# Kernel optimization log

Measured on AMD Instinct MI355X. Metric: run time of the kernel, lower is better.

Reference implementation:

```python
import jax, jax.numpy as jnp
import numpy as np

N = 50000      # nodes per graph
E = 800000     # edges per graph (avg degree 16)
IN = 128       # in_channels == hidden_channels
HID = 128      # out_channels (heads=1)
R = 8          # num_relations
NEG = 0.2      # PyG RGATConv default negative_slope


def setup_inputs() -> dict:
    key = jax.random.key(0)
    ks = jax.random.split(key, 14)
    s_w = (2.0 / (IN + HID)) ** 0.5  # glorot-ish scale
    return {
        "x_one": jax.random.normal(ks[0], (N, IN), jnp.float32),
        "edge_index_one": jax.random.randint(ks[1], (2, E), 0, N),
        "edge_type_one": jax.random.randint(ks[2], (E,), 0, R),
        "x_two": jax.random.normal(ks[3], (N, IN), jnp.float32),
        "edge_index_two": jax.random.randint(ks[4], (2, E), 0, N),
        "edge_type_two": jax.random.randint(ks[5], (E,), 0, R),
        "W1": jax.random.normal(ks[6], (R, IN, HID), jnp.float32) * s_w,
        "q1": jax.random.normal(ks[7], (HID, 1), jnp.float32) * s_w,
        "k1": jax.random.normal(ks[8], (HID, 1), jnp.float32) * s_w,
        "b1": jnp.zeros((HID,), jnp.float32),
        "W2": jax.random.normal(ks[9], (R, IN, HID), jnp.float32) * s_w,
        "q2": jax.random.normal(ks[10], (HID, 1), jnp.float32) * s_w,
        "k2": jax.random.normal(ks[11], (HID, 1), jnp.float32) * s_w,
        "b2": jnp.zeros((HID,), jnp.float32),
    }


def _rgat(x, edge_index, edge_type, W, q, k, b):
    """PyG RGATConv (heads=1, additive-self-attention, across-relation)."""
    n = x.shape[0]
    src, dst = edge_index[0], edge_index[1]
    # per-relation linear transform of all nodes: [R, N, HID]
    xt = jnp.einsum('nd,rdo->rno', x, W)
    out_i = xt[edge_type, dst]   # [E, HID] transformed target (x_i W_r)
    out_j = xt[edge_type, src]   # [E, HID] transformed source (x_j W_r)
    qi = out_i @ q               # [E, 1]
    kj = out_j @ k               # [E, 1]
    alpha = jax.nn.leaky_relu(qi + kj, NEG)
    # scatter-softmax over incoming edges of each dst node
    amax = jax.ops.segment_max(alpha, dst, num_segments=n)
    amax = jnp.where(jnp.isfinite(amax), amax, 0.0)
    ex = jnp.exp(alpha - amax[dst])
    denom = jax.ops.segment_sum(ex, dst, num_segments=n) + 1e-16
    a = ex / denom[dst]          # [E, 1]
    # weighted scatter-add aggregation + bias
    out = jax.ops.segment_sum(a * out_j, dst, num_segments=n) + b
    return out


def reference(x_one, edge_index_one, edge_type_one,
              x_two, edge_index_two, edge_type_two,
              W1, q1, k1, b1, W2, q2, k2, b2):
    o1 = jax.nn.relu(_rgat(x_one, edge_index_one, edge_type_one, W1, q1, k1, b1))
    o2 = jax.nn.relu(_rgat(x_two, edge_index_two, edge_type_two, W2, q2, k2, b2))
    return (o1, o2)
```

## Files before the change

### kernel.cpp

```cpp
#include <hip/hip_runtime.h>


typedef unsigned short u16;
typedef __attribute__((ext_vector_type(8))) short short8;
typedef __attribute__((ext_vector_type(4))) float floatx4;
typedef __attribute__((ext_vector_type(4))) float float4v;
typedef __attribute__((ext_vector_type(4))) unsigned uint4v;

__device__ __forceinline__ u16 f2bf(float f) {
  union { float f; unsigned u; } v; v.f = f;
  unsigned r = v.u + 0x7FFFu + ((v.u >> 16) & 1u);
  return (u16)(r >> 16);
}
__device__ __forceinline__ float bflo(unsigned v) {
  union { unsigned u; float f; } c; c.u = v << 16; return c.f;
}
__device__ __forceinline__ float bfhi(unsigned v) {
  union { unsigned u; float f; } c; c.u = v & 0xffff0000u; return c.f;
}
__device__ __forceinline__ unsigned cvtpk(float lo, float hi) {
  unsigned r;
  asm("v_cvt_pk_bf16_f32 %0, %1, %2" : "=v"(r) : "v"(lo), "v"(hi));
  return r;
}

__global__ void k_prep_wb(const float* __restrict__ W1, const float* __restrict__ W2,
                          u16* __restrict__ Wb, int KK) {
  int t = blockIdx.x * 256 + threadIdx.x;
  int lane = t & 63, nt = (t >> 6) & 7, kk = t >> 9;
  if (kk >= KK) return;
  const float* W = blockIdx.y ? W2 : W1;
  u16* out = Wb + (size_t)blockIdx.y * KK * 4096;
  int q = lane >> 4, m16 = lane & 15;
  int c = nt * 16 + m16;
  short8 v;
#pragma unroll
  for (int j = 0; j < 8; ++j) {
    int k = kk * 32 + q * 8 + j;
    v[j] = (short)f2bf(W[(size_t)k * 128 + c]);
  }
  *(short8*)(out + (size_t)t * 8) = v;
}

__global__ void __launch_bounds__(256) k_prep_bqk(
    const float* __restrict__ W1, const float* __restrict__ q1,
    const float* __restrict__ k1, const float* __restrict__ W2,
    const float* __restrict__ q2, const float* __restrict__ k2,
    u16* __restrict__ Bqk) {
  int idx = blockIdx.x * 256 + threadIdx.x;
  int j = idx & 7, lane = (idx >> 3) & 63, kk = (idx >> 9) & 3, g = idx >> 11;
  int k = kk * 32 + ((lane >> 4) & 3) * 8 + j;
  int n = lane & 15;
  const float* W = g ? W2 : W1;
  const float* vec = (n < 8) ? (g ? q2 : q1) : (g ? k2 : k1);
  const float* row = W + ((size_t)(n & 7) * 128 + k) * 128;
  float s = 0.f;
#pragma unroll
  for (int o = 0; o < 128; o += 4) {
    float4v wv = *(const float4v*)(row + o);
    float4v qv = *(const float4v*)(vec + o);
    s += wv.x * qv.x + wv.y * qv.y + wv.z * qv.z + wv.w * qv.w;
  }
  Bqk[idx] = f2bf(s);
}

__global__ void __launch_bounds__(256) k_count(
    const int* __restrict__ d1, const int* __restrict__ d2,
    int* __restrict__ gcnt, int N, int E, int NB) {
  __shared__ int h[512];
  int tid = threadIdx.x;
  for (int i = tid; i < NB; i += 256) h[i] = 0;
  __syncthreads();
  int E2 = 2 * E;
  int e0 = blockIdx.x * 4096;
#pragma unroll
  for (int j = 0; j < 16; ++j) {
    int e = e0 + j * 256 + tid;
    if (e < E2) {
      int g = e >= E;
      int d = g ? d2[e - E] : d1[e];
      atomicAdd(&h[(g * N + d) >> 8], 1);
    }
  }
  __syncthreads();
  for (int i = tid; i < NB; i += 256)
    if (h[i]) atomicAdd(&gcnt[i], h[i]);
}

__global__ void k_bucket_scan(const int* __restrict__ gcnt, int* __restrict__ bbase,
                              int* __restrict__ bcur, int* __restrict__ offs,
                              int NB, int total, int N2) {
  __shared__ int sd[512];
  int tid = threadIdx.x;
  int v0 = (tid < NB) ? gcnt[tid] : 0;
  int v1 = (tid + 256 < NB) ? gcnt[tid + 256] : 0;
  sd[tid] = v0; sd[tid + 256] = v1;
  __syncthreads();
  for (int off = 1; off < 512; off <<= 1) {
    int t0 = (tid >= off) ? sd[tid - off] : 0;
    int t1 = (tid + 256 >= off) ? sd[tid + 256 - off] : 0;
    __syncthreads();
    sd[tid] += t0; sd[tid + 256] += t1;
    __syncthreads();
  }
  if (tid < NB) { int b = sd[tid] - v0; bbase[tid] = b; bcur[tid] = b; }
  if (tid + 256 < NB) { int b = sd[tid + 256] - v1; bbase[tid + 256] = b; bcur[tid + 256] = b; }
  if (tid == 0) { bbase[NB] = total; offs[N2] = total; }
}

__global__ void __launch_bounds__(256) k_bin(
    const int* __restrict__ ei1, const int* __restrict__ et1,
    const int* __restrict__ ei2, const int* __restrict__ et2,
    int* __restrict__ bcur, uint2* __restrict__ staged, int N, int E, int NB) {
  __shared__ int hist[512];
  __shared__ int basev[512];
  __shared__ int runstart[512];
  __shared__ unsigned sta[4096 * 2];
  int tid = threadIdx.x;
  int E2 = 2 * E;
  int e0 = blockIdx.x * 4096;
  int cnt2 = min(4096, E2 - e0);
  for (int i = tid; i < 512; i += 256) hist[i] = 0;
  __syncthreads();
  int dstg[16], srcet[16], rank[16];
#pragma unroll
  for (int j = 0; j < 16; ++j) {
    int e = e0 + j * 256 + tid;
    dstg[j] = -1;
    if (e < E2) {
      int g = e >= E;
      int el = e - (g ? E : 0);
      const int* ei = g ? ei2 : ei1;
      int s = ei[el], d = ei[E + el];
      int etv = (g ? et2 : et1)[el];
      dstg[j] = g * N + d;
      srcet[j] = (s << 3) | etv;
      rank[j] = atomicAdd(&hist[dstg[j] >> 8], 1);
    }
  }
  __syncthreads();
  basev[tid] = hist[tid];
  basev[tid + 256] = hist[tid + 256];
  __syncthreads();
  for (int off = 1; off < 512; off <<= 1) {
    int i0 = tid, i1 = tid + 256;
    int v0 = (i0 >= off) ? basev[i0 - off] : 0;
    int v1 = (i1 >= off) ? basev[i1 - off] : 0;
    __syncthreads();
    basev[i0] += v0; basev[i1] += v1;
    __syncthreads();
  }
  for (int i = tid; i < NB; i += 256)
    if (hist[i] > 0) runstart[i] = atomicAdd(&bcur[i], hist[i]);
  __syncthreads();
#pragma unroll
  for (int j = 0; j < 16; ++j)
    if (dstg[j] >= 0) {
      int b = dstg[j] >> 8;
      int slot = basev[b] - hist[b] + rank[j];
      sta[slot * 2] = (unsigned)dstg[j];
      sta[slot * 2 + 1] = (unsigned)srcet[j];
    }
  __syncthreads();
  for (int i = tid; i < cnt2; i += 256) {
    unsigned dg = sta[i * 2], se = sta[i * 2 + 1];
    int b = (int)(dg >> 8);
    int dest = runstart[b] + (i - (basev[b] - hist[b]));
    staged[dest] = make_uint2(dg, se);
  }
}

__global__ void __launch_bounds__(256) k_scatter2(
    const uint2* __restrict__ staged, const int* __restrict__ bbase,
    int* __restrict__ offs, int* __restrict__ csr, int N2) {
  __shared__ int hist[256];
  __shared__ int sd[256];
  __shared__ int cur[256];
  int b = blockIdx.x, tid = threadIdx.x;
  int nb0 = b << 8;
  int nnode = min(256, N2 - nb0);
  int s0 = bbase[b], s1 = bbase[b + 1];
  hist[tid] = 0;
  __syncthreads();
  for (int i = s0 + tid; i < s1; i += 256)
    atomicAdd(&hist[(int)staged[i].x - nb0], 1);
  __syncthreads();
  int v = hist[tid];
  sd[tid] = v; __syncthreads();
  for (int off = 1; off < 256; off <<= 1) {
    int t = (tid >= off) ? sd[tid - off] : 0;
    __syncthreads();
    sd[tid] += t;
    __syncthreads();
  }
  int ex = sd[tid] - v;
  if (tid < nnode) offs[nb0 + tid] = s0 + ex;
  cur[tid] = ex;
  __syncthreads();
  for (int i = s0 + tid; i < s1; i += 256) {
    uint2 en = staged[i];
    int node = (int)en.x - nb0;
    int sl = atomicAdd(&cur[node], 1);
    csr[s0 + sl] = (int)en.y;
  }
}

__global__ void __launch_bounds__(256) k_gemm_xt(
    const float* __restrict__ x1, const float* __restrict__ x2,
    const u16* __restrict__ Wb, const u16* __restrict__ Bqk,
    u16* __restrict__ xt, unsigned long long xt_gstride,
    float* __restrict__ sq, float* __restrict__ sk,
    int N, int R, int g0) {
  __shared__ u16 st[4][2][2048];
  int g = g0 + blockIdx.z;
  const float* x = g ? x2 : x1;
  const u16* Wbg = Wb + (size_t)g * (R * 4) * 4096;
  const u16* Bqkg = Bqk + (size_t)g * 2048;
  u16* xtg = xt + (size_t)g * xt_gstride;
  int node_base = g * N;
  int wave = threadIdx.x >> 6, lane = threadIdx.x & 63;
  int m0 = blockIdx.x * 64 + wave * 16;
  int rbase = blockIdx.y * 4;
  int q = lane >> 4, m16 = lane & 15;
  int node = m0 + m16;
  int srow = (node < N) ? node : N - 1;
  short8 bfrag[4];
#pragma unroll
  for (int kk = 0; kk < 4; ++kk) {
    const float* ap = x + (size_t)srow * 128 + kk * 32 + q * 8;
    float4v f0 = *(const float4v*)ap;
    float4v f1 = *(const float4v*)(ap + 4);
    union { unsigned u[4]; short8 s; } pb;
    pb.u[0] = cvtpk(f0.x, f0.y); pb.u[1] = cvtpk(f0.z, f0.w);
    pb.u[2] = cvtpk(f1.x, f1.y); pb.u[3] = cvtpk(f1.z, f1.w);
    bfrag[kk] = pb.s;
  }
  if (blockIdx.y == 0) {
    floatx4 accq = (floatx4){0.f, 0.f, 0.f, 0.f};
#pragma unroll
    for (int kk = 0; kk < 4; ++kk) {
      short8 aq = *(const short8*)(Bqkg + (size_t)kk * 512 + lane * 8);
      accq = __builtin_amdgcn_mfma_f32_16x16x32_bf16(aq, bfrag[kk], accq, 0, 0, 0);
    }
    if (node < N) {
      float* dst = (q < 2 ? sq : sk) + (size_t)(node_base + node) * 8 + (q & 1) * 4;
      *(float4v*)dst = (float4v){accq[0], accq[1], accq[2], accq[3]};
    }
  }
#pragma unroll
  for (int rr = 0; rr < 4; ++rr) {
    int r = rbase + rr;
    u16* s = st[wave][rr & 1];
    floatx4 acc[8];
#pragma unroll
    for (int nt = 0; nt < 8; ++nt) acc[nt] = (floatx4){0.f, 0.f, 0.f, 0.f};
#pragma unroll
    for (int kk = 0; kk < 4; ++kk) {
      const u16* wbp = Wbg + ((size_t)((r * 4 + kk) * 8) * 64 + lane) * 8;
#pragma unroll
      for (int nt = 0; nt < 8; ++nt) {
        short8 a = *(const short8*)(wbp + nt * 512);
        acc[nt] = __builtin_amdgcn_mfma_f32_16x16x32_bf16(a, bfrag[kk], acc[nt], 0, 0, 0);
      }
    }
#pragma unroll
    for (int nt = 0; nt < 8; ++nt) {
      union { unsigned u[2]; unsigned long long ull; } pk;
      pk.u[0] = cvtpk(acc[nt][0], acc[nt][1]);
      pk.u[1] = cvtpk(acc[nt][2], acc[nt][3]);
      int c16 = 2 * nt + (q >> 1);
      *(unsigned long long*)(s + (((m16 << 4) + (c16 ^ m16)) << 3) + ((q & 1) << 2)) = pk.ull;
    }
#pragma unroll
    for (int it = 0; it < 4; ++it) {
      int rl = it * 4 + q;
      int gm = m0 + rl;
      if (gm < N) {
        uint4v vv = *(const uint4v*)(s + (((rl << 4) + (m16 ^ rl)) << 3));
        *(uint4v*)(xtg + ((size_t)r * N + gm) * 128 + m16 * 8) = vv;
      }
    }
  }
}

__global__ void __launch_bounds__(256) k_aggregate(
    const int* __restrict__ csr, const int* __restrict__ offs,
    const float* __restrict__ sq, const float* __restrict__ sk,
    const u16* __restrict__ xt, unsigned long long xt_gstride,
    const float* __restrict__ b1, const float* __restrict__ b2,
    float* __restrict__ out, int N, int g0) {
  int nl = blockIdx.x * 4 + (threadIdx.x >> 6);
  int lane = threadIdx.x & 63;
  if (nl >= N) return;
  int g = g0 + blockIdx.y;
  int node_base = g * N;
  const float* bias = g ? b2 : b1;
  const u16* xtg = xt + (size_t)g * xt_gstride;
  float* outp = out + (size_t)g * N * 128;
  int node = node_base + nl;
  int start = offs[node], end = offs[node + 1];
  const float* sqn = sq + (size_t)node * 8;

  float al[8]; int pl[8];
  float m = -INFINITY;
  {
    int c = 0;
    for (int i = start + lane; i < end; i += 64, ++c) {
      int p = csr[i]; int s = p >> 3, e = p & 7;
      float a = sqn[e] + sk[(size_t)(node_base + s) * 8 + e];
      a = (a > 0.f) ? a : 0.2f * a;
      if (c < 8) { al[c] = a; pl[c] = p; }
      m = fmaxf(m, a);
    }
  }
#pragma unroll
  for (int off = 32; off; off >>= 1) m = fmaxf(m, __shfl_xor(m, off));

  float ssum = 0.f;
  {
    int c = 0;
    for (int i = start + lane; i < end; i += 64, ++c) {
      float a;
      if (c < 8) a = al[c];
      else {
        int p = csr[i]; int s = p >> 3, e = p & 7;
        a = sqn[e] + sk[(size_t)(node_base + s) * 8 + e];
        a = (a > 0.f) ? a : 0.2f * a;
      }
      ssum += __expf(a - m);
    }
  }
#pragma unroll
  for (int off = 32; off; off >>= 1) ssum += __shfl_xor(ssum, off);
  float inv = 1.f / (ssum + 1e-16f);

  float acc0 = 0.f, acc1 = 0.f;
  const char* xtb = (const char*)xtg;
  int c = 0;
  for (int base = start; base < end; base += 64, ++c) {
    int cnt = min(64, end - base);
    float w = 0.f; int b = 0;
    {
      int i = base + lane;
      if (i < end) {
        int p; float a;
        if (c < 8) { p = pl[c]; a = al[c]; }
        else {
          p = csr[i]; int s = p >> 3, e = p & 7;
          a = sqn[e] + sk[(size_t)(node_base + s) * 8 + e];
          a = (a > 0.f) ? a : 0.2f * a;
        }
        w = __expf(a - m) * inv;
        b = ((p & 7) * N + (p >> 3)) << 8;
      }
    }
    int j = 0;
    for (; j + 3 < cnt; j += 4) {
      float w0 = __shfl(w, j), w1 = __shfl(w, j + 1),
            w2 = __shfl(w, j + 2), w3 = __shfl(w, j + 3);
      int b0 = __shfl(b, j), b1_ = __shfl(b, j + 1),
          b2_ = __shfl(b, j + 2), b3 = __shfl(b, j + 3);
      unsigned v0 = *(const unsigned*)(xtb + b0 + lane * 4);
      unsigned v1 = *(const unsigned*)(xtb + b1_ + lane * 4);
      unsigned v2 = *(const unsigned*)(xtb + b2_ + lane * 4);
      unsigned v3 = *(const unsigned*)(xtb + b3 + lane * 4);
      acc0 += w0 * bflo(v0); acc1 += w0 * bfhi(v0);
      acc0 += w1 * bflo(v1); acc1 += w1 * bfhi(v1);
      acc0 += w2 * bflo(v2); acc1 += w2 * bfhi(v2);
      acc0 += w3 * bflo(v3); acc1 += w3 * bfhi(v3);
    }
    for (; j < cnt; ++j) {
      float w0 = __shfl(w, j);
      int b0 = __shfl(b, j);
      unsigned v0 = *(const unsigned*)(xtb + b0 + lane * 4);
      acc0 += w0 * bflo(v0); acc1 += w0 * bfhi(v0);
    }
  }
  float o0 = fmaxf(acc0 + bias[lane * 2], 0.f);
  float o1 = fmaxf(acc1 + bias[lane * 2 + 1], 0.f);
  union { float f[2]; unsigned long long u; } pk;
  pk.f[0] = o0; pk.f[1] = o1;
  __builtin_nontemporal_store(pk.u,
      (unsigned long long*)(outp + (size_t)nl * 128 + lane * 2));
}

extern "C" void kernel_launch(void* const* d_in, const int* in_sizes, int n_in,
                              void* d_out, int out_size, void* d_ws, size_t ws_size,
                              hipStream_t stream) {
  const float* x1 = (const float*)d_in[0];
  const int* ei1 = (const int*)d_in[1];
  const int* et1 = (const int*)d_in[2];
  const float* x2 = (const float*)d_in[3];
  const int* ei2 = (const int*)d_in[4];
  const int* et2 = (const int*)d_in[5];
  const float* W1 = (const float*)d_in[6];
  const float* q1 = (const float*)d_in[7];
  const float* k1 = (const float*)d_in[8];
  const float* b1 = (const float*)d_in[9];
  const float* W2 = (const float*)d_in[10];
  const float* q2 = (const float*)d_in[11];
  const float* k2 = (const float*)d_in[12];
  const float* b2 = (const float*)d_in[13];

  const int N = in_sizes[0] / 128;
  const int E = in_sizes[1] / 2;
  const int R = in_sizes[6] / (128 * 128);
  const int KK = R * 4;
  const int N2 = 2 * N;
  const int NB = (N2 + 255) >> 8;

  size_t off = 0;
  char* w = (char*)d_ws;
  auto carve = [&](size_t bytes) -> void* {
    void* p = w + off;
    off += (bytes + 255) & ~(size_t)255;
    return p;
  };
  u16* Wb = (u16*)carve((size_t)2 * KK * 4096 * 2);
  u16* Bqk = (u16*)carve((size_t)2 * 4 * 64 * 8 * 2);
  float* sq = (float*)carve((size_t)N2 * 8 * 4);
  float* sk = (float*)carve((size_t)N2 * 8 * 4);
  int* offs = (int*)carve((size_t)(N2 + 1) * 4);
  int* gcnt = (int*)carve(512 * 4);
  int* bbase = (int*)carve(520 * 4);
  int* bcur = (int*)carve(512 * 4);
  int* csr = (int*)carve((size_t)2 * E * 4);
  size_t xt_elems = (size_t)R * N * 128;
  u16* xt = (u16*)(w + off);
  bool merged = (off + 2 * xt_elems * 2) <= ws_size;
  if (off + xt_elems * 2 > ws_size) return;
  uint2* staged = (uint2*)xt;
  unsigned long long gstride = merged ? (unsigned long long)xt_elems : 0ull;

  const int nbin = (2 * E + 4095) / 4096;

  hipMemsetAsync(gcnt, 0, 512 * 4, stream);
  k_prep_wb<<<dim3((KK * 512 + 255) / 256, 2), dim3(256), 0, stream>>>(W1, W2, Wb, KK);
  k_prep_bqk<<<dim3(16), dim3(256), 0, stream>>>(W1, q1, k1, W2, q2, k2, Bqk);
  k_count<<<dim3(nbin), dim3(256), 0, stream>>>(ei1 + E, ei2 + E, gcnt, N, E, NB);
  k_bucket_scan<<<dim3(1), dim3(256), 0, stream>>>(gcnt, bbase, bcur, offs, NB, 2 * E, N2);
  k_bin<<<dim3(nbin), dim3(256), 0, stream>>>(ei1, et1, ei2, et2, bcur, staged, N, E, NB);
  k_scatter2<<<dim3(NB), dim3(256), 0, stream>>>(staged, bbase, offs, csr, N2);

  if (merged) {
    k_gemm_xt<<<dim3((N + 63) / 64, 2, 2), dim3(256), 0, stream>>>(
        x1, x2, Wb, Bqk, xt, gstride, sq, sk, N, R, 0);
    k_aggregate<<<dim3((N + 3) / 4, 2), dim3(256), 0, stream>>>(
        csr, offs, sq, sk, xt, gstride, b1, b2, (float*)d_out, N, 0);
  } else {
    for (int g = 0; g < 2; ++g) {
      k_gemm_xt<<<dim3((N + 63) / 64, 2, 1), dim3(256), 0, stream>>>(
          x1, x2, Wb, Bqk, xt, 0ull, sq, sk, N, R, g);
      k_aggregate<<<dim3((N + 3) / 4, 1), dim3(256), 0, stream>>>(
          csr, offs, sq, sk, xt, 0ull, b1, b2, (float*)d_out, N, g);
    }
  }
}
```

Measured before the change: 362.5 us.

## Fuse CSR build stages into one cooperative kernel with grid syncs

```diff
diff --git a/kernel.cpp b/kernel.cpp
--- a/kernel.cpp
+++ b/kernel.cpp
@@ -1,4 +1,7 @@
 #include <hip/hip_runtime.h>
+#include <hip/hip_cooperative_groups.h>
+
+namespace cg = cooperative_groups;
 
 
 typedef unsigned short u16;
@@ -62,6 +65,133 @@
     s += wv.x * qv.x + wv.y * qv.y + wv.z * qv.z + wv.w * qv.w;
   }
   Bqk[idx] = f2bf(s);
+}
+
+__global__ void __launch_bounds__(256) k_sort(
+    const int* __restrict__ ei1, const int* __restrict__ et1,
+    const int* __restrict__ ei2, const int* __restrict__ et2,
+    int* __restrict__ gcnt, int* __restrict__ bbase, int* __restrict__ bcur,
+    int* __restrict__ offs, uint2* __restrict__ staged, int* __restrict__ csr,
+    int N, int E, int NB, int N2, int total) {
+  __shared__ int hist[512];
+  __shared__ int basev[512];
+  __shared__ int runstart[512];
+  __shared__ unsigned sta[4096 * 2];
+  cg::grid_group grid = cg::this_grid();
+  int tid = threadIdx.x;
+  int E2 = 2 * E;
+  int e0 = blockIdx.x * 4096;
+  bool has_edges = (e0 < E2);
+  int cnt2 = has_edges ? min(4096, E2 - e0) : 0;
+
+  for (int i = tid; i < 512; i += 256) hist[i] = 0;
+  __syncthreads();
+  int dstg[16], srcet[16], rank[16];
+#pragma unroll
+  for (int j = 0; j < 16; ++j) dstg[j] = -1;
+  if (has_edges) {
+#pragma unroll
+    for (int j = 0; j < 16; ++j) {
+      int e = e0 + j * 256 + tid;
+      if (e < E2) {
+        int g = e >= E;
+        int el = e - (g ? E : 0);
+        const int* ei = g ? ei2 : ei1;
+        int s = ei[el], d = ei[E + el];
+        int etv = (g ? et2 : et1)[el];
+        dstg[j] = g * N + d;
+        srcet[j] = (s << 3) | etv;
+        rank[j] = atomicAdd(&hist[dstg[j] >> 8], 1);
+      }
+    }
+    __syncthreads();
+    for (int i = tid; i < NB; i += 256)
+      if (hist[i]) atomicAdd(&gcnt[i], hist[i]);
+  }
+  __threadfence();
+  grid.sync();
+
+  if (blockIdx.x == 0) {
+    int v0 = (tid < NB) ? gcnt[tid] : 0;
+    int v1 = (tid + 256 < NB) ? gcnt[tid + 256] : 0;
+    basev[tid] = v0; basev[tid + 256] = v1;
+    __syncthreads();
+    for (int off = 1; off < 512; off <<= 1) {
+      int t0 = (tid >= off) ? basev[tid - off] : 0;
+      int t1 = (tid + 256 >= off) ? basev[tid + 256 - off] : 0;
+      __syncthreads();
+      basev[tid] += t0; basev[tid + 256] += t1;
+      __syncthreads();
+    }
+    if (tid < NB) { int b = basev[tid] - v0; bbase[tid] = b; bcur[tid] = b; }
+    if (tid + 256 < NB) { int b = basev[tid + 256] - v1; bbase[tid + 256] = b; bcur[tid + 256] = b; }
+    if (tid == 0) { bbase[NB] = total; offs[N2] = total; }
+  }
+  __threadfence();
+  grid.sync();
+
+  if (has_edges) {
+    basev[tid] = hist[tid];
+    basev[tid + 256] = hist[tid + 256];
+    __syncthreads();
+    for (int off = 1; off < 512; off <<= 1) {
+      int v0 = (tid >= off) ? basev[tid - off] : 0;
+      int v1 = (tid + 256 >= off) ? basev[tid + 256 - off] : 0;
+      __syncthreads();
+      basev[tid] += v0; basev[tid + 256] += v1;
+      __syncthreads();
+    }
+    for (int i = tid; i < NB; i += 256)
+      if (hist[i] > 0) runstart[i] = atomicAdd(&bcur[i], hist[i]);
+    __syncthreads();
+#pragma unroll
+    for (int j = 0; j < 16; ++j)
+      if (dstg[j] >= 0) {
+        int b = dstg[j] >> 8;
+        int slot = basev[b] - hist[b] + rank[j];
+        sta[slot * 2] = (unsigned)dstg[j];
+        sta[slot * 2 + 1] = (unsigned)srcet[j];
+      }
+    __syncthreads();
+    for (int i = tid; i < cnt2; i += 256) {
+      unsigned dg = sta[i * 2], se = sta[i * 2 + 1];
+      int b = (int)(dg >> 8);
+      int dest = runstart[b] + (i - (basev[b] - hist[b]));
+      staged[dest] = make_uint2(dg, se);
+    }
+  }
+  __threadfence();
+  grid.sync();
+
+  if ((int)blockIdx.x < NB) {
+    int nb0 = blockIdx.x << 8;
+    int nnode = min(256, N2 - nb0);
+    int s0 = bbase[blockIdx.x], s1 = bbase[blockIdx.x + 1];
+    hist[tid] = 0;
+    __syncthreads();
+    for (int i = s0 + tid; i < s1; i += 256)
+      atomicAdd(&hist[(int)staged[i].x - nb0], 1);
+    __syncthreads();
+    int v = hist[tid];
+    basev[tid] = v;
+    __syncthreads();
+    for (int off = 1; off < 256; off <<= 1) {
+      int t = (tid >= off) ? basev[tid - off] : 0;
+      __syncthreads();
+      basev[tid] += t;
+      __syncthreads();
+    }
+    int ex = basev[tid] - v;
+    if (tid < nnode) offs[nb0 + tid] = s0 + ex;
+    runstart[tid] = ex;
+    __syncthreads();
+    for (int i = s0 + tid; i < s1; i += 256) {
+      uint2 en = staged[i];
+      int node = (int)en.x - nb0;
+      int sl = atomicAdd(&runstart[node], 1);
+      csr[s0 + sl] = (int)en.y;
+    }
+  }
 }
 
 __global__ void __launch_bounds__(256) k_count(
@@ -433,14 +563,28 @@
   unsigned long long gstride = merged ? (unsigned long long)xt_elems : 0ull;
 
   const int nbin = (2 * E + 4095) / 4096;
+  const int nblk = nbin > NB ? nbin : NB;
+  int total = 2 * E;
 
   hipMemsetAsync(gcnt, 0, 512 * 4, stream);
   k_prep_wb<<<dim3((KK * 512 + 255) / 256, 2), dim3(256), 0, stream>>>(W1, W2, Wb, KK);
   k_prep_bqk<<<dim3(16), dim3(256), 0, stream>>>(W1, q1, k1, W2, q2, k2, Bqk);
-  k_count<<<dim3(nbin), dim3(256), 0, stream>>>(ei1 + E, ei2 + E, gcnt, N, E, NB);
-  k_bucket_scan<<<dim3(1), dim3(256), 0, stream>>>(gcnt, bbase, bcur, offs, NB, 2 * E, N2);
-  k_bin<<<dim3(nbin), dim3(256), 0, stream>>>(ei1, et1, ei2, et2, bcur, staged, N, E, NB);
-  k_scatter2<<<dim3(NB), dim3(256), 0, stream>>>(staged, bbase, offs, csr, N2);
+
+  {
+    void* args[] = {(void*)&ei1, (void*)&et1, (void*)&ei2, (void*)&et2,
+                    (void*)&gcnt, (void*)&bbase, (void*)&bcur, (void*)&offs,
+                    (void*)&staged, (void*)&csr,
+                    (void*)&N, (void*)&E, (void*)&NB, (void*)&N2, (void*)&total};
+    hipError_t err = hipLaunchCooperativeKernel(
+        (void*)k_sort, dim3(nblk), dim3(256), args, 0, stream);
+    if (err != hipSuccess) {
+      (void)hipGetLastError();
+      k_count<<<dim3(nbin), dim3(256), 0, stream>>>(ei1 + E, ei2 + E, gcnt, N, E, NB);
+      k_bucket_scan<<<dim3(1), dim3(256), 0, stream>>>(gcnt, bbase, bcur, offs, NB, total, N2);
+      k_bin<<<dim3(nbin), dim3(256), 0, stream>>>(ei1, et1, ei2, et2, bcur, staged, N, E, NB);
+      k_scatter2<<<dim3(NB), dim3(256), 0, stream>>>(staged, bbase, offs, csr, N2);
+    }
+  }
 
   if (merged) {
     k_gemm_xt<<<dim3((N + 63) / 64, 2, 2), dim3(256), 0, stream>>>(
```

After: 606.9 us. 1.67x slower.

## Use fixed-capacity buckets to drop count and scan passes in CSR build

Applied to the files above, without the earlier changes.

```diff
diff --git a/kernel.cpp b/kernel.cpp
--- a/kernel.cpp
+++ b/kernel.cpp
@@ -6,6 +6,8 @@
 typedef __attribute__((ext_vector_type(4))) float floatx4;
 typedef __attribute__((ext_vector_type(4))) float float4v;
 typedef __attribute__((ext_vector_type(4))) unsigned uint4v;
+
+#define BCAP 8192
 
 __device__ __forceinline__ u16 f2bf(float f) {
   union { float f; unsigned u; } v; v.f = f;
@@ -64,54 +66,10 @@
   Bqk[idx] = f2bf(s);
 }
 
-__global__ void __launch_bounds__(256) k_count(
-    const int* __restrict__ d1, const int* __restrict__ d2,
-    int* __restrict__ gcnt, int N, int E, int NB) {
-  __shared__ int h[512];
-  int tid = threadIdx.x;
-  for (int i = tid; i < NB; i += 256) h[i] = 0;
-  __syncthreads();
-  int E2 = 2 * E;
-  int e0 = blockIdx.x * 4096;
-#pragma unroll
-  for (int j = 0; j < 16; ++j) {
-    int e = e0 + j * 256 + tid;
-    if (e < E2) {
-      int g = e >= E;
-      int d = g ? d2[e - E] : d1[e];
-      atomicAdd(&h[(g * N + d) >> 8], 1);
-    }
-  }
-  __syncthreads();
-  for (int i = tid; i < NB; i += 256)
-    if (h[i]) atomicAdd(&gcnt[i], h[i]);
-}
-
-__global__ void k_bucket_scan(const int* __restrict__ gcnt, int* __restrict__ bbase,
-                              int* __restrict__ bcur, int* __restrict__ offs,
-                              int NB, int total, int N2) {
-  __shared__ int sd[512];
-  int tid = threadIdx.x;
-  int v0 = (tid < NB) ? gcnt[tid] : 0;
-  int v1 = (tid + 256 < NB) ? gcnt[tid + 256] : 0;
-  sd[tid] = v0; sd[tid + 256] = v1;
-  __syncthreads();
-  for (int off = 1; off < 512; off <<= 1) {
-    int t0 = (tid >= off) ? sd[tid - off] : 0;
-    int t1 = (tid + 256 >= off) ? sd[tid + 256 - off] : 0;
-    __syncthreads();
-    sd[tid] += t0; sd[tid + 256] += t1;
-    __syncthreads();
-  }
-  if (tid < NB) { int b = sd[tid] - v0; bbase[tid] = b; bcur[tid] = b; }
-  if (tid + 256 < NB) { int b = sd[tid + 256] - v1; bbase[tid + 256] = b; bcur[tid + 256] = b; }
-  if (tid == 0) { bbase[NB] = total; offs[N2] = total; }
-}
-
-__global__ void __launch_bounds__(256) k_bin(
+__global__ void __launch_bounds__(256) k_bin2(
     const int* __restrict__ ei1, const int* __restrict__ et1,
     const int* __restrict__ ei2, const int* __restrict__ et2,
-    int* __restrict__ bcur, uint2* __restrict__ staged, int N, int E, int NB) {
+    int* __restrict__ bcnt, uint2* __restrict__ staged, int N, int E, int NB) {
   __shared__ int hist[512];
   __shared__ int basev[512];
   __shared__ int runstart[512];
@@ -151,7 +109,7 @@
     __syncthreads();
   }
   for (int i = tid; i < NB; i += 256)
-    if (hist[i] > 0) runstart[i] = atomicAdd(&bcur[i], hist[i]);
+    if (hist[i] > 0) runstart[i] = atomicAdd(&bcnt[i], hist[i]);
   __syncthreads();
 #pragma unroll
   for (int j = 0; j < 16; ++j)
@@ -165,25 +123,27 @@
   for (int i = tid; i < cnt2; i += 256) {
     unsigned dg = sta[i * 2], se = sta[i * 2 + 1];
     int b = (int)(dg >> 8);
-    int dest = runstart[b] + (i - (basev[b] - hist[b]));
+    int dest = (b << 13) + runstart[b] + (i - (basev[b] - hist[b]));
     staged[dest] = make_uint2(dg, se);
   }
 }
 
-__global__ void __launch_bounds__(256) k_scatter2(
-    const uint2* __restrict__ staged, const int* __restrict__ bbase,
-    int* __restrict__ offs, int* __restrict__ csr, int N2) {
+__global__ void __launch_bounds__(256) k_scatter3(
+    const uint2* __restrict__ staged, const int* __restrict__ bcnt,
+    int* __restrict__ offs, int* __restrict__ ends, int* __restrict__ csr,
+    int N2) {
   __shared__ int hist[256];
   __shared__ int sd[256];
   __shared__ int cur[256];
   int b = blockIdx.x, tid = threadIdx.x;
   int nb0 = b << 8;
   int nnode = min(256, N2 - nb0);
-  int s0 = bbase[b], s1 = bbase[b + 1];
+  int s0 = b << 13;
+  int cnt = bcnt[b];
   hist[tid] = 0;
   __syncthreads();
-  for (int i = s0 + tid; i < s1; i += 256)
-    atomicAdd(&hist[(int)staged[i].x - nb0], 1);
+  for (int i = tid; i < cnt; i += 256)
+    atomicAdd(&hist[(int)staged[s0 + i].x - nb0], 1);
   __syncthreads();
   int v = hist[tid];
   sd[tid] = v; __syncthreads();
@@ -194,11 +154,14 @@
     __syncthreads();
   }
   int ex = sd[tid] - v;
-  if (tid < nnode) offs[nb0 + tid] = s0 + ex;
+  if (tid < nnode) {
+    offs[nb0 + tid] = s0 + ex;
+    ends[nb0 + tid] = s0 + ex + v;
+  }
   cur[tid] = ex;
   __syncthreads();
-  for (int i = s0 + tid; i < s1; i += 256) {
-    uint2 en = staged[i];
+  for (int i = tid; i < cnt; i += 256) {
+    uint2 en = staged[s0 + i];
     int node = (int)en.x - nb0;
     int sl = atomicAdd(&cur[node], 1);
     csr[s0 + sl] = (int)en.y;
@@ -206,18 +169,11 @@
 }
 
 __global__ void __launch_bounds__(256) k_gemm_xt(
-    const float* __restrict__ x1, const float* __restrict__ x2,
-    const u16* __restrict__ Wb, const u16* __restrict__ Bqk,
-    u16* __restrict__ xt, unsigned long long xt_gstride,
+    const float* __restrict__ x, const u16* __restrict__ Wb,
+    const u16* __restrict__ Bqk, u16* __restrict__ xt,
     float* __restrict__ sq, float* __restrict__ sk,
-    int N, int R, int g0) {
+    int N, int R, int node_base) {
   __shared__ u16 st[4][2][2048];
-  int g = g0 + blockIdx.z;
-  const float* x = g ? x2 : x1;
-  const u16* Wbg = Wb + (size_t)g * (R * 4) * 4096;
-  const u16* Bqkg = Bqk + (size_t)g * 2048;
-  u16* xtg = xt + (size_t)g * xt_gstride;
-  int node_base = g * N;
   int wave = threadIdx.x >> 6, lane = threadIdx.x & 63;
   int m0 = blockIdx.x * 64 + wave * 16;
   int rbase = blockIdx.y * 4;
@@ -239,7 +195,7 @@
     floatx4 accq = (floatx4){0.f, 0.f, 0.f, 0.f};
 #pragma unroll
     for (int kk = 0; kk < 4; ++kk) {
-      short8 aq = *(const short8*)(Bqkg + (size_t)kk * 512 + lane * 8);
+      short8 aq = *(const short8*)(Bqk + (size_t)kk * 512 + lane * 8);
       accq = __builtin_amdgcn_mfma_f32_16x16x32_bf16(aq, bfrag[kk], accq, 0, 0, 0);
     }
     if (node < N) {
@@ -256,7 +212,7 @@
     for (int nt = 0; nt < 8; ++nt) acc[nt] = (floatx4){0.f, 0.f, 0.f, 0.f};
 #pragma unroll
     for (int kk = 0; kk < 4; ++kk) {
-      const u16* wbp = Wbg + ((size_t)((r * 4 + kk) * 8) * 64 + lane) * 8;
+      const u16* wbp = Wb + ((size_t)((r * 4 + kk) * 8) * 64 + lane) * 8;
 #pragma unroll
       for (int nt = 0; nt < 8; ++nt) {
         short8 a = *(const short8*)(wbp + nt * 512);
@@ -277,7 +233,7 @@
       int gm = m0 + rl;
       if (gm < N) {
         uint4v vv = *(const uint4v*)(s + (((rl << 4) + (m16 ^ rl)) << 3));
-        *(uint4v*)(xtg + ((size_t)r * N + gm) * 128 + m16 * 8) = vv;
+        *(uint4v*)(xt + ((size_t)r * N + gm) * 128 + m16 * 8) = vv;
       }
     }
   }
@@ -285,20 +241,15 @@
 
 __global__ void __launch_bounds__(256) k_aggregate(
     const int* __restrict__ csr, const int* __restrict__ offs,
+    const int* __restrict__ ends,
     const float* __restrict__ sq, const float* __restrict__ sk,
-    const u16* __restrict__ xt, unsigned long long xt_gstride,
-    const float* __restrict__ b1, const float* __restrict__ b2,
-    float* __restrict__ out, int N, int g0) {
+    const u16* __restrict__ xt, const float* __restrict__ bias,
+    float* __restrict__ out, int N, int node_base) {
   int nl = blockIdx.x * 4 + (threadIdx.x >> 6);
   int lane = threadIdx.x & 63;
   if (nl >= N) return;
-  int g = g0 + blockIdx.y;
-  int node_base = g * N;
-  const float* bias = g ? b2 : b1;
-  const u16* xtg = xt + (size_t)g * xt_gstride;
-  float* outp = out + (size_t)g * N * 128;
   int node = node_base + nl;
-  int start = offs[node], end = offs[node + 1];
+  int start = offs[node], end = ends[node];
   const float* sqn = sq + (size_t)node * 8;
 
   float al[8]; int pl[8];
@@ -335,7 +286,7 @@
   float inv = 1.f / (ssum + 1e-16f);
 
   float acc0 = 0.f, acc1 = 0.f;
-  const char* xtb = (const char*)xtg;
+  const char* xtb = (const char*)xt;
   int c = 0;
   for (int base = start; base < end; base += 64, ++c) {
     int cnt = min(64, end - base);
@@ -358,11 +309,11 @@
     for (; j + 3 < cnt; j += 4) {
       float w0 = __shfl(w, j), w1 = __shfl(w, j + 1),
             w2 = __shfl(w, j + 2), w3 = __shfl(w, j + 3);
-      int b0 = __shfl(b, j), b1_ = __shfl(b, j + 1),
-          b2_ = __shfl(b, j + 2), b3 = __shfl(b, j + 3);
+      int b0 = __shfl(b, j), b1 = __shfl(b, j + 1),
+          b2 = __shfl(b, j + 2), b3 = __shfl(b, j + 3);
       unsigned v0 = *(const unsigned*)(xtb + b0 + lane * 4);
-      unsigned v1 = *(const unsigned*)(xtb + b1_ + lane * 4);
-      unsigned v2 = *(const unsigned*)(xtb + b2_ + lane * 4);
+      unsigned v1 = *(const unsigned*)(xtb + b1 + lane * 4);
+      unsigned v2 = *(const unsigned*)(xtb + b2 + lane * 4);
       unsigned v3 = *(const unsigned*)(xtb + b3 + lane * 4);
       acc0 += w0 * bflo(v0); acc1 += w0 * bfhi(v0);
       acc0 += w1 * bflo(v1); acc1 += w1 * bfhi(v1);
@@ -381,7 +332,7 @@
   union { float f[2]; unsigned long long u; } pk;
   pk.f[0] = o0; pk.f[1] = o1;
   __builtin_nontemporal_store(pk.u,
-      (unsigned long long*)(outp + (size_t)nl * 128 + lane * 2));
+      (unsigned long long*)(out + (size_t)nl * 128 + lane * 2));
 }
 
 extern "C" void kernel_launch(void* const* d_in, const int* in_sizes, int n_in,
@@ -420,39 +371,31 @@
   u16* Bqk = (u16*)carve((size_t)2 * 4 * 64 * 8 * 2);
   float* sq = (float*)carve((size_t)N2 * 8 * 4);
   float* sk = (float*)carve((size_t)N2 * 8 * 4);
-  int* offs = (int*)carve((size_t)(N2 + 1) * 4);
-  int* gcnt = (int*)carve(512 * 4);
-  int* bbase = (int*)carve(520 * 4);
-  int* bcur = (int*)carve(512 * 4);
-  int* csr = (int*)carve((size_t)2 * E * 4);
-  size_t xt_elems = (size_t)R * N * 128;
-  u16* xt = (u16*)(w + off);
-  bool merged = (off + 2 * xt_elems * 2) <= ws_size;
-  if (off + xt_elems * 2 > ws_size) return;
+  int* offs = (int*)carve((size_t)N2 * 4);
+  int* ends = (int*)carve((size_t)N2 * 4);
+  int* bcnt = (int*)carve(512 * 4);
+  int* csr = (int*)carve((size_t)NB * BCAP * 4);
+  u16* xt = (u16*)carve((size_t)R * N * 128 * 2);
   uint2* staged = (uint2*)xt;
-  unsigned long long gstride = merged ? (unsigned long long)xt_elems : 0ull;
+  if (off > ws_size) return;
+  if ((size_t)NB * BCAP * 8 > (size_t)R * N * 128 * 2) return;
 
   const int nbin = (2 * E + 4095) / 4096;
 
-  hipMemsetAsync(gcnt, 0, 512 * 4, stream);
+  hipMemsetAsync(bcnt, 0, 512 * 4, stream);
   k_prep_wb<<<dim3((KK * 512 + 255) / 256, 2), dim3(256), 0, stream>>>(W1, W2, Wb, KK);
   k_prep_bqk<<<dim3(16), dim3(256), 0, stream>>>(W1, q1, k1, W2, q2, k2, Bqk);
-  k_count<<<dim3(nbin), dim3(256), 0, stream>>>(ei1 + E, ei2 + E, gcnt, N, E, NB);
-  k_bucket_scan<<<dim3(1), dim3(256), 0, stream>>>(gcnt, bbase, bcur, offs, NB, 2 * E, N2);
-  k_bin<<<dim3(nbin), dim3(256), 0, stream>>>(ei1, et1, ei2, et2, bcur, staged, N, E, NB);
-  k_scatter2<<<dim3(NB), dim3(256), 0, stream>>>(staged, bbase, offs, csr, N2);
-
-  if (merged) {
-    k_gemm_xt<<<dim3((N + 63) / 64, 2, 2), dim3(256), 0, stream>>>(
-        x1, x2, Wb, Bqk, xt, gstride, sq, sk, N, R, 0);
-    k_aggregate<<<dim3((N + 3) / 4, 2), dim3(256), 0, stream>>>(
-        csr, offs, sq, sk, xt, gstride, b1, b2, (float*)d_out, N, 0);
-  } else {
-    for (int g = 0; g < 2; ++g) {
-      k_gemm_xt<<<dim3((N + 63) / 64, 2, 1), dim3(256), 0, stream>>>(
-          x1, x2, Wb, Bqk, xt, 0ull, sq, sk, N, R, g);
-      k_aggregate<<<dim3((N + 3) / 4, 1), dim3(256), 0, stream>>>(
-          csr, offs, sq, sk, xt, 0ull, b1, b2, (float*)d_out, N, g);
-    }
-  }
-}
+  k_bin2<<<dim3(nbin), dim3(256), 0, stream>>>(ei1, et1, ei2, et2, bcnt, staged, N, E, NB);
+  k_scatter3<<<dim3(NB), dim3(256), 0, stream>>>(staged, bcnt, offs, ends, csr, N2);
+
+  for (int g = 0; g < 2; ++g) {
+    const float* x = g ? x2 : x1;
+    const float* bv = g ? b2 : b1;
+    float* outp = (float*)d_out + (size_t)g * N * 128;
+    k_gemm_xt<<<dim3((N + 63) / 64, 2), dim3(256), 0, stream>>>(
+        x, Wb + (size_t)g * KK * 4096, Bqk + (size_t)g * 2048, xt,
+        sq, sk, N, R, g * N);
+    k_aggregate<<<dim3((N + 3) / 4), dim3(256), 0, stream>>>(
+        csr, offs, ends, sq, sk, xt, bv, outp, N, g * N);
+  }
+}
```

Result: faster. 340.9 us (-6.0%).
